# Optimization experiments

Hardware: AMD Instinct MI355X
Metric: run time of the kernel (lower is better)

## Reference

```python
import jax, jax.numpy as jnp
import numpy as np

G = 16        # groups / heads
DG = 128      # per-group dim (2048/16)
F = 2048      # feat dim (representation_size)
N = 2048      # num_rois
M = 2048      # num_nongt_rois


def setup_inputs() -> dict:
    key = jax.random.key(0)
    ks = jax.random.split(key, 8)
    std = np.float32(0.02)
    return {
        "roi_feat": jax.random.normal(ks[0], (N, F), jnp.float32),
        "ref_feat": jax.random.normal(ks[1], (M, F), jnp.float32),
        "Wq_w": jax.random.normal(ks[2], (F, F), jnp.float32) * std,
        "Wq_b": jnp.zeros((F,), jnp.float32),
        "Wk_w": jax.random.normal(ks[3], (F, F), jnp.float32) * std,
        "Wk_b": jnp.zeros((F,), jnp.float32),
        # grouped 1x1 conv weight [2048, 2048, 1, 1] squeezed to [F, F];
        # group g maps input channels [g*F_g_in] -> output channels [g*DG:(g+1)*DG]
        "Wv_w": jax.random.normal(ks[4], (F, F), jnp.float32) * np.float32(0.01),
        "Wv_b": jnp.zeros((F,), jnp.float32),
    }


def reference(roi_feat, ref_feat, Wq_w, Wq_b, Wk_w, Wk_b, Wv_w, Wv_b):
    n = roi_feat.shape[0]
    scale = np.float32(1.0 / np.sqrt(DG))
    # torch Linear: y = x @ W.T + b
    q = (roi_feat @ Wq_w.T + Wq_b).reshape(n, G, DG)      # [N, G, DG]
    k = (ref_feat @ Wk_w.T + Wk_b).reshape(-1, G, DG)     # [M, G, DG]
    aff = jnp.einsum("ngd,mgd->ngm", q, k) * scale        # [N, G, M]
    attn = jax.nn.softmax(aff, axis=-1)
    # weighted values: v is raw ref_feat, per original
    ov = jnp.einsum("ngm,mf->ngf", attn, ref_feat)        # [N, G, F]
    # grouped 1x1 conv: per-group linear F -> DG
    Wv3 = Wv_w.reshape(G, DG, F)                          # [G, DG, F]
    out = jnp.einsum("ngf,gdf->ngd", ov, Wv3) + Wv_b.reshape(G, DG)
    return out.reshape(n, G * DG)                          # [N, F]
```

## Files before the change

### kernel.cpp

```cpp
#include <hip/hip_runtime.h>
#include <hip/hip_bf16.h>

#define G_   16
#define DG_  128
#define F_   2048
#define N_   2048
#define M_   2048

typedef __attribute__((ext_vector_type(8))) short s16x8;
typedef __attribute__((ext_vector_type(4))) float f32x4;
typedef __attribute__((ext_vector_type(2))) unsigned int u32x2;

typedef const __attribute__((address_space(1))) void GV;
typedef __attribute__((address_space(3))) void LV;

__device__ inline unsigned short f2bf(float f) {
  unsigned u = __float_as_uint(f);
  u += 0x7fffu + ((u >> 16) & 1u);
  return (unsigned short)(u >> 16);
}

struct Cvt5Args { const float* s[5]; unsigned short* d[5]; };

__global__ __launch_bounds__(256)
void cvt5(Cvt5Args a) {
  unsigned u = blockIdx.x * 256 + threadIdx.x;
  if (u >= 5u * 524288u) return;
  int seg = u >> 19;
  unsigned off = u & 524287u;
  const float4* sp = (const float4*)(a.s[seg] + (size_t)off * 8);
  float4 x = sp[0], y = sp[1];
  uint4 o;
  o.x = (unsigned)f2bf(x.x) | ((unsigned)f2bf(x.y) << 16);
  o.y = (unsigned)f2bf(x.z) | ((unsigned)f2bf(x.w) << 16);
  o.z = (unsigned)f2bf(y.x) | ((unsigned)f2bf(y.y) << 16);
  o.w = (unsigned)f2bf(y.z) | ((unsigned)f2bf(y.w) << 16);
  *(uint4*)(a.d[seg] + (size_t)off * 8) = o;
}

struct GemmJobs {
  const unsigned short* A[3];
  const unsigned short* B[3];
  const float* bias[3];
  unsigned short* C[3];
  float osc[3];
};

__global__ __launch_bounds__(512, 2)
void gemm8(GemmJobs jb) {
  __shared__ __align__(16) char lds[131072];
  const int j  = blockIdx.x >> 6;
  const int bs = blockIdx.x & 63;
  const unsigned short* A = jb.A[j];
  const unsigned short* B = jb.B[j];
  const float* bias = jb.bias[j];
  unsigned short* C = jb.C[j];
  const float osc = jb.osc[j];

  const int tid = threadIdx.x, lane = tid & 63, wv = tid >> 6;
  const int wm = wv >> 2, wn = wv & 3;
  const int l15 = lane & 15, l4 = lane >> 4;
  const int m0 = (bs >> 3) * 256, n0 = (bs & 7) * 256;
  const int xo  = (l15 & 7) << 4;
  const int ksw = ((lane & 7) ^ (lane >> 3)) * 8;
  const int brr0 = (wn & 1) * 64;

  f32x4 acc[8][4];
#pragma unroll
  for (int i = 0; i < 8; ++i)
#pragma unroll
    for (int nf = 0; nf < 4; ++nf) acc[i][nf] = (f32x4){0.f, 0.f, 0.f, 0.f};

  auto stage_half = [&](int buf2, const unsigned short* Mat, int lbase,
                        int h, int row0, int k0) {
#pragma unroll
    for (int c = 0; c < 2; ++c) {
      __builtin_amdgcn_global_load_lds(
          (GV*)(Mat + (size_t)(row0 + h * 128 + c * 64 + wv * 8 + (lane >> 3)) * F_
                + k0 + ksw),
          (LV*)(lds + buf2 * 65536 + lbase + h * 16384 + c * 8192 + wv * 1024),
          16, 0, 0);
    }
  };

  stage_half(0, A, 0,     0, m0, 0);
  stage_half(0, A, 0,     1, m0, 0);
  stage_half(0, B, 32768, 0, n0, 0);
  stage_half(0, B, 32768, 1, n0, 0);
  asm volatile("s_waitcnt vmcnt(0)" ::: "memory");
  __builtin_amdgcn_sched_barrier(0);
  __builtin_amdgcn_s_barrier();

  const int NT = F_ / 64;
  for (int t = 0; t < NT; ++t) {
    const int buf = t & 1;
    const char* Ab = lds + buf * 65536 + wm * 16384;
    const char* Bb = lds + buf * 65536 + 32768 + (wn >> 1) * 16384;
    const bool pf = (t + 1 < NT);
    const int k1 = (t + 1) * 64;
    s16x8 af[4], bf[4];

    auto ldA = [&](int mf, int ks) {
      return *(const s16x8*)(Ab + (mf * 16 + l15) * 128 + ((ks * 64 + l4 * 16) ^ xo));
    };
    auto ldB = [&](int nf, int ks) {
      return *(const s16x8*)(Bb + (brr0 + nf * 16 + l15) * 128 + ((ks * 64 + l4 * 16) ^ xo));
    };

#pragma unroll
    for (int nf = 0; nf < 4; ++nf) bf[nf] = ldB(nf, 0);
#pragma unroll
    for (int i = 0; i < 4; ++i) af[i] = ldA(i, 0);
    if (pf) stage_half(buf ^ 1, A, 0, 0, m0, k1);
    __builtin_amdgcn_sched_barrier(0);
    __builtin_amdgcn_s_barrier();
    asm volatile("s_waitcnt lgkmcnt(0)" ::: "memory");
    __builtin_amdgcn_sched_barrier(0);
    __builtin_amdgcn_s_setprio(1);
#pragma unroll
    for (int i = 0; i < 4; ++i)
#pragma unroll
      for (int nf = 0; nf < 4; ++nf)
        acc[i][nf] = __builtin_amdgcn_mfma_f32_16x16x32_bf16(af[i], bf[nf], acc[i][nf], 0, 0, 0);
    __builtin_amdgcn_s_setprio(0);
    __builtin_amdgcn_sched_barrier(0);
    __builtin_amdgcn_s_barrier();

#pragma unroll
    for (int i = 0; i < 4; ++i) af[i] = ldA(4 + i, 0);
    if (pf) stage_half(buf ^ 1, A, 0, 1, m0, k1);
    __builtin_amdgcn_sched_barrier(0);
    __builtin_amdgcn_s_barrier();
    asm volatile("s_waitcnt lgkmcnt(0)" ::: "memory");
    __builtin_amdgcn_sched_barrier(0);
    __builtin_amdgcn_s_setprio(1);
#pragma unroll
    for (int i = 0; i < 4; ++i)
#pragma unroll
      for (int nf = 0; nf < 4; ++nf)
        acc[4 + i][nf] = __builtin_amdgcn_mfma_f32_16x16x32_bf16(af[i], bf[nf], acc[4 + i][nf], 0, 0, 0);
    __builtin_amdgcn_s_setprio(0);
    __builtin_amdgcn_sched_barrier(0);
    __builtin_amdgcn_s_barrier();

#pragma unroll
    for (int nf = 0; nf < 4; ++nf) bf[nf] = ldB(nf, 1);
#pragma unroll
    for (int i = 0; i < 4; ++i) af[i] = ldA(i, 1);
    if (pf) stage_half(buf ^ 1, B, 32768, 0, n0, k1);
    __builtin_amdgcn_sched_barrier(0);
    __builtin_amdgcn_s_barrier();
    asm volatile("s_waitcnt lgkmcnt(0)" ::: "memory");
    __builtin_amdgcn_sched_barrier(0);
    __builtin_amdgcn_s_setprio(1);
#pragma unroll
    for (int i = 0; i < 4; ++i)
#pragma unroll
      for (int nf = 0; nf < 4; ++nf)
        acc[i][nf] = __builtin_amdgcn_mfma_f32_16x16x32_bf16(af[i], bf[nf], acc[i][nf], 0, 0, 0);
    __builtin_amdgcn_s_setprio(0);
    __builtin_amdgcn_sched_barrier(0);
    __builtin_amdgcn_s_barrier();

#pragma unroll
    for (int i = 0; i < 4; ++i) af[i] = ldA(4 + i, 1);
    if (pf) stage_half(buf ^ 1, B, 32768, 1, n0, k1);
    __builtin_amdgcn_sched_barrier(0);
    __builtin_amdgcn_s_barrier();
    asm volatile("s_waitcnt lgkmcnt(0)" ::: "memory");
    __builtin_amdgcn_sched_barrier(0);
    __builtin_amdgcn_s_setprio(1);
#pragma unroll
    for (int i = 0; i < 4; ++i)
#pragma unroll
      for (int nf = 0; nf < 4; ++nf)
        acc[4 + i][nf] = __builtin_amdgcn_mfma_f32_16x16x32_bf16(af[i], bf[nf], acc[4 + i][nf], 0, 0, 0);
    __builtin_amdgcn_s_setprio(0);
    asm volatile("s_waitcnt vmcnt(0)" ::: "memory");
    __builtin_amdgcn_sched_barrier(0);
    __builtin_amdgcn_s_barrier();
  }

#pragma unroll
  for (int nf = 0; nf < 4; ++nf) {
    int c = n0 + wn * 64 + nf * 16 + l15;
    float bv = bias ? bias[c] : 0.f;
#pragma unroll
    for (int mf = 0; mf < 8; ++mf) {
#pragma unroll
      for (int jj = 0; jj < 4; ++jj) {
        int r = m0 + wm * 128 + mf * 16 + l4 * 4 + jj;
        C[(size_t)r * F_ + c] = f2bf((acc[mf][nf][jj] + bv) * osc);
      }
    }
  }
}

__global__ __launch_bounds__(256, 2)
void attn_mfma(const unsigned short* __restrict__ Q,
               const unsigned short* __restrict__ K,
               const unsigned short* __restrict__ Vt,
               const float* __restrict__ vb,
               float* __restrict__ out) {
  __shared__ unsigned short Kt[2][64 * 128];
  __shared__ unsigned short Vts[2][128 * 64];
  __shared__ unsigned short Pt[4][16 * 64];
  const int tid = threadIdx.x, lane = tid & 63, wv = tid >> 6;
  const int l15 = lane & 15, l4 = lane >> 4;
  const int g = blockIdx.y;
  const int q0 = blockIdx.x * 64 + wv * 16;

  s16x8 qa[4];
#pragma unroll
  for (int kc = 0; kc < 4; ++kc)
    qa[kc] = *(const s16x8*)(Q + (size_t)(q0 + l15) * F_ + g * DG_ + kc * 32 + l4 * 8);

  f32x4 oa[8];
#pragma unroll
  for (int df = 0; df < 8; ++df) oa[df] = (f32x4){0.f, 0.f, 0.f, 0.f};
  float m_r = -1e30f, l_r = 0.f;

  const int ksw0 = (((lane & 15) ^ (lane >> 4)) * 8);
  const int ksw1 = (((lane & 15) ^ 4 ^ (lane >> 4)) * 8);
  const int vsw  = (((lane & 7) ^ (lane >> 3)) * 8);
  const int xorb = (l15 & 7) << 4;
  int csw[4];
#pragma unroll
  for (int kc = 0; kc < 4; ++kc) csw[kc] = (kc * 64 + l4 * 16) ^ xorb;

  auto stage = [&](int buf, int kv0) {
#pragma unroll
    for (int i = 0; i < 4; ++i) {
      int r0 = wv * 16 + i * 4;
      __builtin_amdgcn_global_load_lds(
          (GV*)(K + (size_t)(kv0 + r0 + (lane >> 4)) * F_ + g * DG_ + ((i & 1) ? ksw1 : ksw0)),
          (LV*)(&Kt[buf][r0 * 128]), 16, 0, 0);
    }
#pragma unroll
    for (int i = 0; i < 4; ++i) {
      int r0 = wv * 32 + i * 8;
      __builtin_amdgcn_global_load_lds(
          (GV*)(Vt + (size_t)(g * DG_ + r0 + (lane >> 3)) * M_ + kv0 + vsw),
          (LV*)(&Vts[buf][r0 * 64]), 16, 0, 0);
    }
  };

  stage(0, 0);
  __syncthreads();
  int cur = 0;
  unsigned short* Pw = &Pt[wv][0];

  for (int t = 0; t < M_ / 64; ++t) {
    if (t + 1 < M_ / 64) stage(cur ^ 1, (t + 1) * 64);
    const unsigned short* Kb = &Kt[cur][0];
    const unsigned short* Vb = &Vts[cur][0];

    f32x4 sf[4];
    __builtin_amdgcn_s_setprio(1);
#pragma unroll
    for (int kvf = 0; kvf < 4; ++kvf) {
      f32x4 s = (f32x4){0.f, 0.f, 0.f, 0.f};
#pragma unroll
      for (int kc = 0; kc < 4; ++kc) {
        s16x8 kf = *(const s16x8*)((const char*)Kb + (kvf * 16 + l15) * 256 + csw[kc]);
        s = __builtin_amdgcn_mfma_f32_16x16x32_bf16(kf, qa[kc], s, 0, 0, 0);
      }
      sf[kvf] = s;
    }
    __builtin_amdgcn_s_setprio(0);

    float tmax = sf[0][0];
#pragma unroll
    for (int kvf = 0; kvf < 4; ++kvf) {
      tmax = fmaxf(tmax, fmaxf(fmaxf(sf[kvf][0], sf[kvf][1]),
                               fmaxf(sf[kvf][2], sf[kvf][3])));
    }
    tmax = fmaxf(tmax, __shfl_xor(tmax, 16));
    tmax = fmaxf(tmax, __shfl_xor(tmax, 32));
    if (!__all(tmax <= m_r + 8.0f)) {
      float mnew = fmaxf(m_r, tmax);
      float corr = __builtin_amdgcn_exp2f(m_r - mnew);
      m_r = mnew;
      l_r *= corr;
      float c0 = __shfl(corr, l4 * 4 + 0);
      float c1 = __shfl(corr, l4 * 4 + 1);
      float c2 = __shfl(corr, l4 * 4 + 2);
      float c3 = __shfl(corr, l4 * 4 + 3);
#pragma unroll
      for (int df = 0; df < 8; ++df) {
        oa[df][0] *= c0; oa[df][1] *= c1; oa[df][2] *= c2; oa[df][3] *= c3;
      }
    }

    float psum = 0.f;
#pragma unroll
    for (int kvf = 0; kvf < 4; ++kvf) {
      float p0 = __builtin_amdgcn_exp2f(sf[kvf][0] - m_r);
      float p1 = __builtin_amdgcn_exp2f(sf[kvf][1] - m_r);
      float p2 = __builtin_amdgcn_exp2f(sf[kvf][2] - m_r);
      float p3 = __builtin_amdgcn_exp2f(sf[kvf][3] - m_r);
      psum += (p0 + p1) + (p2 + p3);
      u32x2 w;
      asm("v_cvt_pk_bf16_f32 %0, %1, %2" : "=v"(w.x) : "v"(p0), "v"(p1));
      asm("v_cvt_pk_bf16_f32 %0, %1, %2" : "=v"(w.y) : "v"(p2), "v"(p3));
      *(u32x2*)((char*)Pw + l15 * 128 + ((kvf * 32 + l4 * 8) ^ xorb)) = w;
    }
    psum += __shfl_xor(psum, 16);
    psum += __shfl_xor(psum, 32);
    l_r += psum;

    s16x8 pa0 = *(const s16x8*)((const char*)Pw + l15 * 128 + csw[0]);
    s16x8 pa1 = *(const s16x8*)((const char*)Pw + l15 * 128 + csw[1]);
    __builtin_amdgcn_s_setprio(1);
#pragma unroll
    for (int df = 0; df < 8; ++df) {
      s16x8 v0 = *(const s16x8*)((const char*)Vb + (df * 16 + l15) * 128 + csw[0]);
      s16x8 v1 = *(const s16x8*)((const char*)Vb + (df * 16 + l15) * 128 + csw[1]);
      oa[df] = __builtin_amdgcn_mfma_f32_16x16x32_bf16(pa0, v0, oa[df], 0, 0, 0);
      oa[df] = __builtin_amdgcn_mfma_f32_16x16x32_bf16(pa1, v1, oa[df], 0, 0, 0);
    }
    __builtin_amdgcn_s_setprio(0);
    __syncthreads();
    cur ^= 1;
  }

  float linv = 1.0f / l_r;
  float i0 = __shfl(linv, l4 * 4 + 0);
  float i1 = __shfl(linv, l4 * 4 + 1);
  float i2 = __shfl(linv, l4 * 4 + 2);
  float i3 = __shfl(linv, l4 * 4 + 3);
#pragma unroll
  for (int df = 0; df < 8; ++df) {
    int c = g * DG_ + df * 16 + l15;
    float bv = vb[c];
    out[(size_t)(q0 + l4 * 4 + 0) * F_ + c] = oa[df][0] * i0 + bv;
    out[(size_t)(q0 + l4 * 4 + 1) * F_ + c] = oa[df][1] * i1 + bv;
    out[(size_t)(q0 + l4 * 4 + 2) * F_ + c] = oa[df][2] * i2 + bv;
    out[(size_t)(q0 + l4 * 4 + 3) * F_ + c] = oa[df][3] * i3 + bv;
  }
}

extern "C" void kernel_launch(void* const* d_in, const int* in_sizes, int n_in,
                              void* d_out, int out_size, void* d_ws, size_t ws_size,
                              hipStream_t stream) {
  const float* roi  = (const float*)d_in[0];
  const float* ref  = (const float*)d_in[1];
  const float* Wq_w = (const float*)d_in[2];
  const float* Wq_b = (const float*)d_in[3];
  const float* Wk_w = (const float*)d_in[4];
  const float* Wk_b = (const float*)d_in[5];
  const float* Wv_w = (const float*)d_in[6];
  const float* Wv_b = (const float*)d_in[7];
  float* out = (float*)d_out;
  const size_t SEG = 4194304;
  const float cscale = 0.12751664508246770f;

  if (ws_size < 64ull * 1024 * 1024) return;
  unsigned short* roi_bf = (unsigned short*)d_ws;
  unsigned short* ref_bf = roi_bf + SEG;
  unsigned short* Wq_bf  = ref_bf + SEG;
  unsigned short* Wk_bf  = Wq_bf + SEG;
  unsigned short* Wv_bf  = Wk_bf + SEG;
  unsigned short* Qb     = Wv_bf + SEG;
  unsigned short* Kb     = Qb + SEG;
  unsigned short* Vtb    = Kb + SEG;

  Cvt5Args ca;
  ca.s[0] = roi;  ca.d[0] = roi_bf;
  ca.s[1] = ref;  ca.d[1] = ref_bf;
  ca.s[2] = Wq_w; ca.d[2] = Wq_bf;
  ca.s[3] = Wk_w; ca.d[3] = Wk_bf;
  ca.s[4] = Wv_w; ca.d[4] = Wv_bf;
  cvt5<<<10240, 256, 0, stream>>>(ca);

  GemmJobs jb;
  jb.A[0] = roi_bf; jb.B[0] = Wq_bf;  jb.bias[0] = Wq_b;    jb.C[0] = Qb;  jb.osc[0] = cscale;
  jb.A[1] = ref_bf; jb.B[1] = Wk_bf;  jb.bias[1] = Wk_b;    jb.C[1] = Kb;  jb.osc[1] = 1.0f;
  jb.A[2] = Wv_bf;  jb.B[2] = ref_bf; jb.bias[2] = nullptr; jb.C[2] = Vtb; jb.osc[2] = 1.0f;
  gemm8<<<192, 512, 0, stream>>>(jb);

  attn_mfma<<<dim3(N_ / 64, G_), 256, 0, stream>>>(Qb, Kb, Vtb, Wv_b, out);
}
```

Before: 141.6 us.

## Split K-halves in LDS, relax vmcnt waits, and remap blocks across XCDs

The GEMM block index is remapped so consecutive blocks spread across the 8 XCDs. The LDS tile layout is reorganized by K-half (32 columns each) with a new XOR swizzle. Staging order becomes A-half0, B-half0, A-half1, B-half1, and the full vmcnt(0) wait is replaced by partial vmcnt(4) waits, so the second K-half load overlaps compute on the first. The goal is to hide global-to-LDS latency and improve L2 locality. The cost is more delicate synchronization correctness.

```diff
diff --git a/kernel.cpp b/kernel.cpp
--- a/kernel.cpp
+++ b/kernel.cpp
@@ -49,8 +49,9 @@
 __global__ __launch_bounds__(512, 2)
 void gemm8(GemmJobs jb) {
   __shared__ __align__(16) char lds[131072];
-  const int j  = blockIdx.x >> 6;
-  const int bs = blockIdx.x & 63;
+  const int wg = (blockIdx.x & 7) * 24 + (blockIdx.x >> 3);
+  const int j  = wg >> 6;
+  const int bs = wg & 63;
   const unsigned short* A = jb.A[j];
   const unsigned short* B = jb.B[j];
   const float* bias = jb.bias[j];
@@ -61,9 +62,11 @@
   const int wm = wv >> 2, wn = wv & 3;
   const int l15 = lane & 15, l4 = lane >> 4;
   const int m0 = (bs >> 3) * 256, n0 = (bs & 7) * 256;
-  const int xo  = (l15 & 7) << 4;
-  const int ksw = ((lane & 7) ^ (lane >> 3)) * 8;
-  const int brr0 = (wn & 1) * 64;
+  const int slot = (l4 ^ (l15 & 3)) * 16;
+  const int scol = (((lane & 3) ^ ((lane >> 2) & 3)) * 8);
+  const int srow = wv * 16 + (lane >> 2);
+  const int rA = wm * 128 + l15;
+  const int rB = (wn >> 1) * 128 + (wn & 1) * 64 + l15;
 
   f32x4 acc[8][4];
 #pragma unroll
@@ -71,47 +74,45 @@
 #pragma unroll
     for (int nf = 0; nf < 4; ++nf) acc[i][nf] = (f32x4){0.f, 0.f, 0.f, 0.f};
 
-  auto stage_half = [&](int buf2, const unsigned short* Mat, int lbase,
-                        int h, int row0, int k0) {
-#pragma unroll
-    for (int c = 0; c < 2; ++c) {
+  auto stage = [&](int buf2, const unsigned short* Mat, int lbase, int h,
+                   int row0, int k0) {
+#pragma unroll
+    for (int rb = 0; rb < 2; ++rb) {
       __builtin_amdgcn_global_load_lds(
-          (GV*)(Mat + (size_t)(row0 + h * 128 + c * 64 + wv * 8 + (lane >> 3)) * F_
-                + k0 + ksw),
-          (LV*)(lds + buf2 * 65536 + lbase + h * 16384 + c * 8192 + wv * 1024),
+          (GV*)(Mat + (size_t)(row0 + rb * 128 + srow) * F_ + k0 + h * 32 + scol),
+          (LV*)(lds + buf2 * 65536 + lbase + h * 16384 + rb * 8192 + wv * 1024),
           16, 0, 0);
     }
   };
 
-  stage_half(0, A, 0,     0, m0, 0);
-  stage_half(0, A, 0,     1, m0, 0);
-  stage_half(0, B, 32768, 0, n0, 0);
-  stage_half(0, B, 32768, 1, n0, 0);
-  asm volatile("s_waitcnt vmcnt(0)" ::: "memory");
+  stage(0, A, 0,     0, m0, 0);
+  stage(0, B, 32768, 0, n0, 0);
+  stage(0, A, 0,     1, m0, 0);
+  stage(0, B, 32768, 1, n0, 0);
+  asm volatile("s_waitcnt vmcnt(4)" ::: "memory");
   __builtin_amdgcn_sched_barrier(0);
   __builtin_amdgcn_s_barrier();
 
   const int NT = F_ / 64;
   for (int t = 0; t < NT; ++t) {
     const int buf = t & 1;
-    const char* Ab = lds + buf * 65536 + wm * 16384;
-    const char* Bb = lds + buf * 65536 + 32768 + (wn >> 1) * 16384;
+    const char* Lb = lds + buf * 65536;
     const bool pf = (t + 1 < NT);
     const int k1 = (t + 1) * 64;
     s16x8 af[4], bf[4];
 
-    auto ldA = [&](int mf, int ks) {
-      return *(const s16x8*)(Ab + (mf * 16 + l15) * 128 + ((ks * 64 + l4 * 16) ^ xo));
+    auto ldA = [&](int mf, int h) {
+      return *(const s16x8*)(Lb + h * 16384 + (rA + mf * 16) * 64 + slot);
     };
-    auto ldB = [&](int nf, int ks) {
-      return *(const s16x8*)(Bb + (brr0 + nf * 16 + l15) * 128 + ((ks * 64 + l4 * 16) ^ xo));
+    auto ldB = [&](int nf, int h) {
+      return *(const s16x8*)(Lb + 32768 + h * 16384 + (rB + nf * 16) * 64 + slot);
     };
 
 #pragma unroll
     for (int nf = 0; nf < 4; ++nf) bf[nf] = ldB(nf, 0);
 #pragma unroll
     for (int i = 0; i < 4; ++i) af[i] = ldA(i, 0);
-    if (pf) stage_half(buf ^ 1, A, 0, 0, m0, k1);
+    if (pf) stage(buf ^ 1, A, 0, 0, m0, k1);
     __builtin_amdgcn_sched_barrier(0);
     __builtin_amdgcn_s_barrier();
     asm volatile("s_waitcnt lgkmcnt(0)" ::: "memory");
@@ -128,7 +129,7 @@
 
 #pragma unroll
     for (int i = 0; i < 4; ++i) af[i] = ldA(4 + i, 0);
-    if (pf) stage_half(buf ^ 1, A, 0, 1, m0, k1);
+    if (pf) stage(buf ^ 1, B, 32768, 0, n0, k1);
     __builtin_amdgcn_sched_barrier(0);
     __builtin_amdgcn_s_barrier();
     asm volatile("s_waitcnt lgkmcnt(0)" ::: "memory");
@@ -140,6 +141,8 @@
       for (int nf = 0; nf < 4; ++nf)
         acc[4 + i][nf] = __builtin_amdgcn_mfma_f32_16x16x32_bf16(af[i], bf[nf], acc[4 + i][nf], 0, 0, 0);
     __builtin_amdgcn_s_setprio(0);
+    if (pf) { asm volatile("s_waitcnt vmcnt(4)" ::: "memory"); }
+    else    { asm volatile("s_waitcnt vmcnt(0)" ::: "memory"); }
     __builtin_amdgcn_sched_barrier(0);
     __builtin_amdgcn_s_barrier();
 
@@ -147,7 +150,7 @@
     for (int nf = 0; nf < 4; ++nf) bf[nf] = ldB(nf, 1);
 #pragma unroll
     for (int i = 0; i < 4; ++i) af[i] = ldA(i, 1);
-    if (pf) stage_half(buf ^ 1, B, 32768, 0, n0, k1);
+    if (pf) stage(buf ^ 1, A, 0, 1, m0, k1);
     __builtin_amdgcn_sched_barrier(0);
     __builtin_amdgcn_s_barrier();
     asm volatile("s_waitcnt lgkmcnt(0)" ::: "memory");
@@ -164,7 +167,7 @@
 
 #pragma unroll
     for (int i = 0; i < 4; ++i) af[i] = ldA(4 + i, 1);
-    if (pf) stage_half(buf ^ 1, B, 32768, 1, n0, k1);
+    if (pf) stage(buf ^ 1, B, 32768, 1, n0, k1);
     __builtin_amdgcn_sched_barrier(0);
     __builtin_amdgcn_s_barrier();
     asm volatile("s_waitcnt lgkmcnt(0)" ::: "memory");
@@ -176,7 +179,7 @@
       for (int nf = 0; nf < 4; ++nf)
         acc[4 + i][nf] = __builtin_amdgcn_mfma_f32_16x16x32_bf16(af[i], bf[nf], acc[4 + i][nf], 0, 0, 0);
     __builtin_amdgcn_s_setprio(0);
-    asm volatile("s_waitcnt vmcnt(0)" ::: "memory");
+    if (pf) { asm volatile("s_waitcnt vmcnt(4)" ::: "memory"); }
     __builtin_amdgcn_sched_barrier(0);
     __builtin_amdgcn_s_barrier();
   }
```

Result: slower. 147.1 us (+3.9%).
